# Optimization experiments

Hardware: AMD Instinct MI355X
Metric: run time of the kernel (lower is better)

Reference implementation:

```python
import jax, jax.numpy as jnp
import numpy as np

N = 100000
E = 1600000
K = 15        # kernel_size (num Gaussian mixture components)
DIM = 3       # pseudo-coordinate dim
EPS = 1e-15   # PyG GMMConv sigma epsilon
BN_EPS = 1e-5
CH = [(50, 75), (75, 100), (100, 75), (75, 50)]


def setup_inputs() -> dict:
    key = jax.random.key(0)
    ks = iter(jax.random.split(key, 64))
    inp = {}
    inp["x"] = jax.random.normal(next(ks), (N, 50), jnp.float32)
    inp["edge_index"] = jax.random.randint(next(ks), (2, E), 0, N, jnp.int64)
    inp["edge_attr"] = jax.random.uniform(next(ks), (E, DIM), jnp.float32)
    for l, (cin, cout) in enumerate(CH, 1):
        inp[f"g{l}"] = jax.random.normal(next(ks), (cin, K, cout), jnp.float32) * 0.1
        inp[f"mu{l}"] = jax.random.normal(next(ks), (K, DIM), jnp.float32)
        inp[f"sigma{l}"] = jnp.ones((K, DIM), jnp.float32) + 0.1 * jax.random.uniform(next(ks), (K, DIM), jnp.float32)
        inp[f"root{l}"] = jax.random.normal(next(ks), (cin, cout), jnp.float32) * 0.1
        inp[f"b{l}"] = jax.random.normal(next(ks), (cout,), jnp.float32) * 0.01
        if l < 4:
            inp[f"gamma{l}"] = jnp.ones((cout,), jnp.float32)
            inp[f"beta{l}"] = jnp.zeros((cout,), jnp.float32)
    return inp


def gmm_layer(x, src, tgt, pseudo, g, mu, sigma, root, bias):
    # Gaussian mixture edge weights: w[e,k] = exp(-0.5 * sum_d (u_ed - mu_kd)^2 / sigma_kd^2)
    n = x.shape[0]
    diff = pseudo[:, None, :] - mu[None, :, :]              # [E,K,dim]
    w = jnp.exp(-0.5 * jnp.sum(diff * diff / (sigma[None] ** 2 + EPS), axis=-1))  # [E,K]
    xs = x[src]                                             # gather source feats [E,Cin]
    # out_t = sum_k (sum_{e->t} w_ek * x_src[e]) @ G_k  (avoids [E,K,Cout] tensor)
    agg = jnp.zeros((n, g.shape[2]), x.dtype)
    for k in range(K):
        zk = jax.ops.segment_sum(xs * w[:, k:k + 1], tgt, num_segments=n)  # [N,Cin]
        agg = agg + zk @ g[:, k, :]
    deg = jax.ops.segment_sum(jnp.ones((src.shape[0],), x.dtype), tgt, num_segments=n)
    agg = agg / jnp.maximum(deg, 1.0)[:, None]              # aggr='mean'
    return agg + x @ root + bias


def batchnorm(x, gamma, beta):
    m = jnp.mean(x, axis=0)
    v = jnp.var(x, axis=0)
    return gamma * (x - m) * jax.lax.rsqrt(v + BN_EPS) + beta


def reference(x, edge_index, edge_attr,
              g1, mu1, sigma1, root1, b1, gamma1, beta1,
              g2, mu2, sigma2, root2, b2, gamma2, beta2,
              g3, mu3, sigma3, root3, b3, gamma3, beta3,
              g4, mu4, sigma4, root4, b4):
    src, tgt = edge_index[0], edge_index[1]
    h = jax.nn.elu(gmm_layer(x, src, tgt, edge_attr, g1, mu1, sigma1, root1, b1))
    h = batchnorm(h, gamma1, beta1)
    h = jax.nn.elu(gmm_layer(h, src, tgt, edge_attr, g2, mu2, sigma2, root2, b2))
    h = batchnorm(h, gamma2, beta2)
    h = jax.nn.elu(gmm_layer(h, src, tgt, edge_attr, g3, mu3, sigma3, root3, b3))
    h = batchnorm(h, gamma3, beta3)
    return gmm_layer(h, src, tgt, edge_attr, g4, mu4, sigma4, root4, b4)
```

## Files before the change

### kernel.cpp

```cpp
#include <hip/hip_runtime.h>
#include <stdint.h>

#define NN 100000
#define NE 1600000
#define KG 15

typedef unsigned short u16;
typedef __attribute__((ext_vector_type(8))) short short8;
typedef __attribute__((ext_vector_type(8))) __bf16 bf16x8;
typedef __attribute__((ext_vector_type(4))) float f32x4;

static __device__ __forceinline__ float bf2f(u16 u){ return __uint_as_float(((unsigned)u)<<16); }
static __device__ __forceinline__ u16 f2bf(float f){
  unsigned u = __float_as_uint(f);
  u += 0x7FFFu + ((u>>16)&1u);
  return (u16)(u>>16);
}
static __device__ __forceinline__ float ldf(const void* p, long long i, int isf32){
  return isf32 ? ((const float*)p)[i] : bf2f(((const u16*)p)[i]);
}
static __device__ __forceinline__ int ld_idx(const void* p, long long i, int isi64){
  return isi64 ? (int)((const long long*)p)[i] : ((const int*)p)[i];
}
static __device__ __forceinline__ f32x4 mfma16x16x32(short8 a, short8 b, f32x4 c){
  return __builtin_amdgcn_mfma_f32_16x16x32_bf16(
      __builtin_bit_cast(bf16x8, a), __builtin_bit_cast(bf16x8, b), c, 0, 0, 0);
}

__global__ void k_sentinel(float* out, float val){
  if (threadIdx.x == 0 && blockIdx.x == 0) out[0] = val;
}

__global__ void k_probe(const void* sg1, const void* ei, int* flags){
  if (threadIdx.x == 0 && blockIdx.x == 0){
    const u16* p = (const u16*)sg1;
    int sane = 1;
    for (int i=0;i<45;i++){ float v = bf2f(p[i]); if (!(v > 0.5f && v < 2.0f)) sane = 0; }
    flags[0] = sane ? 0 : 1;
    const int* q = (const int*)ei;
    int allz = 1;
    for (int i=1;i<128;i+=2) if (q[i] != 0) allz = 0;
    flags[1] = allz ? 1 : 0;
  }
}

__global__ __launch_bounds__(256) void k_convx(const void* x, u16* xcv, const int* flags){
  int i = blockIdx.x*256 + threadIdx.x;
  int c = i & 63, r = i >> 6;
  if (r >= NN) return;
  int isf = flags[0];
  u16 v = 0;
  if (c < 50){
    long long s = (long long)r*50 + c;
    v = isf ? f2bf(((const float*)x)[s]) : ((const u16*)x)[s];
  }
  xcv[(size_t)r*64 + c] = v;
}

__global__ __launch_bounds__(256) void k_deg(const void* ei, int* __restrict__ deg, const int* flags){
  int e = blockIdx.x*256 + threadIdx.x;
  int isi64 = flags[1];
  atomicAdd(&deg[ld_idx(ei, (long long)NE + e, isi64)], 1);
}

__global__ __launch_bounds__(256) void k_scan1(const int* __restrict__ deg, int* __restrict__ rp,
                                               int* __restrict__ bsum){
  __shared__ int lds[256];
  int b = blockIdx.x, t = threadIdx.x;
  int base = b*1024 + t*4;
  int v[4]; int s = 0;
  #pragma unroll
  for (int i=0;i<4;i++){ v[i] = (base+i < NN) ? deg[base+i] : 0; s += v[i]; }
  lds[t] = s; __syncthreads();
  int inc = s;
  for (int off=1; off<256; off<<=1){
    int y = (t>=off) ? lds[t-off] : 0;
    __syncthreads();
    inc += y; lds[t] = inc;
    __syncthreads();
  }
  int excl = inc - s;
  #pragma unroll
  for (int i=0;i<4;i++){ if (base+i < NN) rp[base+i] = excl; excl += v[i]; }
  if (t == 255) bsum[b] = inc;
}

__global__ __launch_bounds__(128) void k_scan2(int* __restrict__ bsum, int* __restrict__ rp){
  __shared__ int lds[128];
  int t = threadIdx.x;
  const int nb = (NN + 1023)/1024;
  int s = (t < nb) ? bsum[t] : 0;
  lds[t] = s; __syncthreads();
  int inc = s;
  for (int off=1; off<128; off<<=1){
    int y = (t>=off) ? lds[t-off] : 0;
    __syncthreads();
    inc += y; lds[t] = inc;
    __syncthreads();
  }
  bsum[t] = inc - s;
  if (t == 0) rp[NN] = NE;
}

__global__ __launch_bounds__(256) void k_scan3(int* __restrict__ rp, const int* __restrict__ bsum){
  int b = blockIdx.x, t = threadIdx.x;
  int add = bsum[b];
  int base = b*1024 + t*4;
  #pragma unroll
  for (int i=0;i<4;i++) if (base+i < NN) rp[base+i] += add;
}

__global__ __launch_bounds__(256) void k_fill(const void* ei, const void* attr,
                                              const int* __restrict__ rp, int* __restrict__ cur,
                                              int* __restrict__ perm, int4* __restrict__ csr16,
                                              int emode, const int* flags){
  int e = blockIdx.x*256 + threadIdx.x;
  int isf = flags[0], isi64 = flags[1];
  int t = ld_idx(ei, (long long)NE + e, isi64);
  int p = rp[t] + atomicAdd(&cur[t], 1);
  if (emode){
    int s = ld_idx(ei, e, isi64);
    float u0 = ldf(attr, 3LL*e+0, isf), u1 = ldf(attr, 3LL*e+1, isf), u2 = ldf(attr, 3LL*e+2, isf);
    csr16[p] = make_int4(s, __float_as_int(u0), __float_as_int(u1), __float_as_int(u2));
  } else {
    perm[p] = e;
  }
}

__global__ __launch_bounds__(256) void k_repack(const void* g, const void* root,
                                                u16* __restrict__ bp, int KC, int CIN, int COUT,
                                                int KS, int NCT, const int* flags){
  int tid = blockIdx.x*256 + threadIdx.x;
  int total = NCT*KS*64;
  if (tid >= total) return;
  int isf = flags[0];
  int lane = tid & 63;
  int ks = (tid >> 6) % KS;
  int ct = tid / (64*KS);
  int c = ct*16 + (lane & 15);
  int kbase = ks*32 + (lane >> 4)*8;
  short8 v8 = {};
  #pragma unroll
  for (int j=0;j<8;j++){
    int kk = kbase + j; u16 v = 0;
    if (c < COUT){
      if (kk < KC){
        int k = kk / CIN, cin = kk - k*CIN;
        v = f2bf(ldf(g, ((long long)cin*KG + k)*COUT + c, isf));
      } else if (kk < KC + CIN){
        v = f2bf(ldf(root, (long long)(kk-KC)*COUT + c, isf));
      }
    }
    v8[j] = (short)v;
  }
  ((short8*)bp)[tid] = v8;
}

template<int CIN, int COUT, int KPAD, int NCT, int XS, bool EM16, bool FINAL>
__global__ __launch_bounds__(512) void k_fused(
    const int4* __restrict__ csr16, const int* __restrict__ perm,
    const void* ei, const void* attr, const int* __restrict__ rp,
    const u16* __restrict__ xin, const void* mu, const void* sg,
    const u16* __restrict__ bp, const void* bias,
    u16* __restrict__ h, float* __restrict__ outp,
    float* __restrict__ sums, float* __restrict__ sumsq, const int* flags)
{
  constexpr int KC   = CIN*KG;
  constexpr int P    = (CIN + 31)/32;
  constexpr int NA   = 2*P;
  constexpr int RS   = KPAD + 8;
  constexpr int KS   = KPAD/32;
  __shared__ short8 zsh[16*RS/8];
  u16* zb = (u16*)zsh;

  int isf = flags[0], isi64 = flags[1];
  int wv = threadIdx.x >> 6, lane = threadIdx.x & 63;
  int m = lane & 15, q = lane >> 4;
  int node0 = blockIdx.x * 16;

  bool kvalid = (m < KG);
  int mm = kvalid ? m : 0;
  float mu0 = ldf(mu, mm*3+0, isf), mu1 = ldf(mu, mm*3+1, isf), mu2 = ldf(mu, mm*3+2, isf);
  float s0 = ldf(sg, mm*3+0, isf),  s1 = ldf(sg, mm*3+1, isf),  s2 = ldf(sg, mm*3+2, isf);
  float is0 = 1.f/(s0*s0 + 1e-15f), is1 = 1.f/(s1*s1 + 1e-15f), is2 = 1.f/(s2*s2 + 1e-15f);

  #pragma unroll 1
  for (int s = 0; s < 2; s++){
    int r = wv*2 + s;
    int t = node0 + r;
    int rs = rp[t], re = rp[t+1];
    f32x4 acc[NA] = {};
    int lastE = re - 1;
    for (int base = rs; base < re; base += 32){
      int e0 = base + q*8;
      int srcs[8];
      short8 af;
      {
        float u0[8], u1[8], u2[8];
        if (EM16){
          int4 ce[8];
          #pragma unroll
          for (int j=0;j<8;j++){
            int ep = e0 + j; ep = (ep > lastE) ? lastE : ep;
            ce[j] = csr16[ep];
          }
          #pragma unroll
          for (int j=0;j<8;j++){
            srcs[j] = ce[j].x;
            u0[j] = __int_as_float(ce[j].y); u1[j] = __int_as_float(ce[j].z); u2[j] = __int_as_float(ce[j].w);
          }
        } else {
          int eix[8];
          #pragma unroll
          for (int j=0;j<8;j++){
            int ep = e0 + j; ep = (ep > lastE) ? lastE : ep;
            eix[j] = perm[ep];
          }
          #pragma unroll
          for (int j=0;j<8;j++) srcs[j] = ld_idx(ei, eix[j], isi64);
          #pragma unroll
          for (int j=0;j<8;j++){
            u0[j] = ldf(attr, 3LL*eix[j]+0, isf);
            u1[j] = ldf(attr, 3LL*eix[j]+1, isf);
            u2[j] = ldf(attr, 3LL*eix[j]+2, isf);
          }
        }
        #pragma unroll
        for (int j=0;j<8;j++){
          float d0 = u0[j] - mu0, d1 = u1[j] - mu1, d2 = u2[j] - mu2;
          float w = __expf(-0.5f*(d0*d0*is0 + d1*d1*is1 + d2*d2*is2));
          bool ok = kvalid && (e0 + j <= lastE);
          w = ok ? w : 0.f;
          af[j] = (short)f2bf(w);
        }
      }

      unsigned xw[8*P];
      #pragma unroll
      for (int p=0; p<P; p++)
        #pragma unroll
        for (int j=0;j<8;j++)
          xw[p*8+j] = *(const unsigned*)(xin + (size_t)srcs[j]*XS + p*32 + 2*m);

      #pragma unroll
      for (int p=0; p<P; p++){
        int cin_e = p*32 + 2*m;
        bool ve = (cin_e < CIN), vo = (cin_e + 1 < CIN);
        short8 bfe, bfo;
        #pragma unroll
        for (int j=0;j<8;j++){
          bfe[j] = ve ? (short)(xw[p*8+j] & 0xffffu) : (short)0;
          bfo[j] = vo ? (short)(xw[p*8+j] >> 16) : (short)0;
        }
        acc[2*p]   = mfma16x16x32(af, bfe, acc[2*p]);
        acc[2*p+1] = mfma16x16x32(af, bfo, acc[2*p+1]);
      }
    }

    int dg = re - rs;
    float inv = 1.f / (float)(dg > 0 ? dg : 1);
    u16* row = zb + r*RS;
    #pragma unroll
    for (int ct=0; ct<NA; ct++){
      int cin = (ct>>1)*32 + 2*m + (ct&1);
      if (cin < CIN){
        #pragma unroll
        for (int rr=0;rr<4;rr++){
          int k = q*4 + rr;
          if (k < KG) row[k*CIN + cin] = f2bf(acc[ct][rr]*inv);
        }
      }
    }
    for (int idx = lane; idx < KPAD - KC; idx += 64){
      u16 v = 0;
      if (idx < CIN) v = xin[(size_t)t*XS + idx];
      row[KC + idx] = v;
    }
  }

  __syncthreads();

  if (wv < NCT){
    const short8* bpv = (const short8*)bp;
    const short8* zv  = (const short8*)zsh;
    f32x4 a0 = {}, a1 = {};
    #pragma unroll 2
    for (int ks=0; ks+1<KS; ks+=2){
      short8 af0 = zv[m*(RS/8) + ks*4 + q];
      short8 bf0 = bpv[(wv*KS + ks)*64 + lane];
      a0 = mfma16x16x32(af0, bf0, a0);
      short8 af1 = zv[m*(RS/8) + (ks+1)*4 + q];
      short8 bf1 = bpv[(wv*KS + ks+1)*64 + lane];
      a1 = mfma16x16x32(af1, bf1, a1);
    }
    if (KS & 1){
      short8 af0 = zv[m*(RS/8) + (KS-1)*4 + q];
      short8 bf0 = bpv[(wv*KS + KS-1)*64 + lane];
      a0 = mfma16x16x32(af0, bf0, a0);
    }
    f32x4 acc = a0 + a1;
    int col = wv*16 + m;
    if (col < COUT){
      float bv = ldf(bias, col, isf);
      float vs[4];
      #pragma unroll
      for (int rr=0;rr<4;rr++){
        int rrow = node0 + q*4 + rr;
        float v = acc[rr] + bv;
        if (!FINAL){
          v = (v > 0.f) ? v : (__expf(v) - 1.f);
          vs[rr] = v;
          h[(size_t)rrow*COUT + col] = f2bf(v);
        } else {
          outp[(size_t)rrow*COUT + col] = v;
        }
      }
      if (!FINAL){
        float ss = vs[0]+vs[1]+vs[2]+vs[3];
        float qq = vs[0]*vs[0]+vs[1]*vs[1]+vs[2]*vs[2]+vs[3]*vs[3];
        ss += __shfl_xor(ss, 16); ss += __shfl_xor(ss, 32);
        qq += __shfl_xor(qq, 16); qq += __shfl_xor(qq, 32);
        if (q == 0){
          atomicAdd(&sums[col], ss);
          atomicAdd(&sumsq[col], qq);
        }
      }
    }
  }
}

__global__ __launch_bounds__(256) void k_bn(const u16* __restrict__ h, const void* gamma,
                                            const void* beta, const float* __restrict__ sums,
                                            const float* __restrict__ sumsq, u16* __restrict__ xo,
                                            int COUT, const int* flags){
  int t = threadIdx.x;
  int isf = flags[0];
  int c = t & 127;
  int r = blockIdx.x*2 + (t >> 7);
  if (r >= NN) return;
  if (c >= COUT){
    if (c < 128) xo[(size_t)r*128 + c] = 0;
    return;
  }
  const float invn = 1.f/(float)NN;
  float mean = sums[c]*invn;
  float var  = sumsq[c]*invn - mean*mean;
  float g = ldf(gamma, c, isf), b = ldf(beta, c, isf);
  float v = g*(bf2f(h[(size_t)r*COUT + c]) - mean)*rsqrtf(var + 1e-5f) + b;
  xo[(size_t)r*128 + c] = f2bf(v);
}

extern "C" void kernel_launch(void* const* d_in, const int* in_sizes, int n_in,
                              void* d_out, int out_size, void* d_ws, size_t ws_size,
                              hipStream_t stream)
{
  static const int expected[29] = {
    5000000, 3200000, 4800000,
    56250, 45, 45, 3750, 75, 75, 75,
    112500, 45, 45, 7500, 100, 100, 100,
    112500, 45, 45, 7500, 75, 75, 75,
    56250, 45, 45, 3750, 50
  };
  if (n_in != 29){ k_sentinel<<<1, 64, 0, stream>>>((float*)d_out, 512.0f); return; }
  for (int j=0;j<29;j++){
    if (in_sizes[j] != expected[j]){
      k_sentinel<<<1, 64, 0, stream>>>((float*)d_out, 1024.0f*(float)(1+j));
      return;
    }
  }

  const void* x0   = d_in[0];
  const void* ei   = d_in[1];
  const void* attr = d_in[2];
  const void* G[4]  = {d_in[3],  d_in[10], d_in[17], d_in[24]};
  const void* MU[4] = {d_in[4],  d_in[11], d_in[18], d_in[25]};
  const void* SG[4] = {d_in[5],  d_in[12], d_in[19], d_in[26]};
  const void* RT[4] = {d_in[6],  d_in[13], d_in[20], d_in[27]};
  const void* BI[4] = {d_in[7],  d_in[14], d_in[21], d_in[28]};
  const void* GA[3] = {d_in[8],  d_in[15], d_in[22]};
  const void* BE[3] = {d_in[9],  d_in[16], d_in[23]};

  char* w = (char*)d_ws;
  auto alloc = [&](size_t bytes)->char*{ char* p = w; w += (bytes + 255) & ~(size_t)255; return p; };
  int*  flags = (int*) alloc(256);
  int*  deg  = (int*) alloc((size_t)NN*4);
  int*  cur  = (int*) alloc((size_t)NN*4);
  int*  rp   = (int*) alloc((size_t)(NN+1)*4);
  int*  bsum = (int*) alloc(512*4);
  u16*  h    = (u16*) alloc((size_t)NN*100*2);
  u16*  xb   = (u16*) alloc((size_t)NN*128*2);
  u16*  bp   = (u16*) alloc(1<<19);
  float* sums  = (float*)alloc(512);
  float* sumsq = (float*)alloc(512);
  u16*  xcv  = xb + (size_t)NN*64;

  size_t base = (size_t)(w - (char*)d_ws);
  int emode; int* perm = nullptr; int4* csr16 = nullptr;
  if (ws_size >= base + (size_t)NE*16 + 4096){
    emode = 1; csr16 = (int4*)alloc((size_t)NE*16);
  } else if (ws_size >= base + (size_t)NE*4 + 4096){
    emode = 0; perm = (int*)alloc((size_t)NE*4);
  } else {
    float mb = (float)(ws_size >> 20); if (mb > 255.f) mb = 255.f;
    k_sentinel<<<1, 64, 0, stream>>>((float*)d_out, 65536.0f + 256.0f*mb);
    return;
  }

  k_probe<<<1, 64, 0, stream>>>(SG[0], ei, flags);
  k_convx<<<NN*64/256, 256, 0, stream>>>(x0, xcv, flags);

  hipMemsetAsync(deg, 0, (size_t)NN*4, stream);
  hipMemsetAsync(cur, 0, (size_t)NN*4, stream);
  k_deg  <<<NE/256, 256, 0, stream>>>(ei, deg, flags);
  k_scan1<<<(NN+1023)/1024, 256, 0, stream>>>(deg, rp, bsum);
  k_scan2<<<1, 128, 0, stream>>>(bsum, rp);
  k_scan3<<<(NN+1023)/1024, 256, 0, stream>>>(rp, bsum);
  k_fill <<<NE/256, 256, 0, stream>>>(ei, attr, rp, cur, perm, csr16, emode, flags);

  const int NB = NN/16;

  {
    k_repack<<<(5*25*64 + 255)/256, 256, 0, stream>>>(G[0], RT[0], bp, 750, 50, 75, 25, 5, flags);
    hipMemsetAsync(sums, 0, 512, stream); hipMemsetAsync(sumsq, 0, 512, stream);
    if (emode) k_fused<50,75,800,5,64,true ,false><<<NB,512,0,stream>>>(csr16, perm, ei, attr, rp, xcv, MU[0], SG[0], bp, BI[0], h, nullptr, sums, sumsq, flags);
    else       k_fused<50,75,800,5,64,false,false><<<NB,512,0,stream>>>(csr16, perm, ei, attr, rp, xcv, MU[0], SG[0], bp, BI[0], h, nullptr, sums, sumsq, flags);
    k_bn<<<NN/2, 256, 0, stream>>>(h, GA[0], BE[0], sums, sumsq, xb, 75, flags);
  }

  {
    k_repack<<<(7*38*64 + 255)/256, 256, 0, stream>>>(G[1], RT[1], bp, 1125, 75, 100, 38, 7, flags);
    hipMemsetAsync(sums, 0, 512, stream); hipMemsetAsync(sumsq, 0, 512, stream);
    if (emode) k_fused<75,100,1216,7,128,true ,false><<<NB,512,0,stream>>>(csr16, perm, ei, attr, rp, xb, MU[1], SG[1], bp, BI[1], h, nullptr, sums, sumsq, flags);
    else       k_fused<75,100,1216,7,128,false,false><<<NB,512,0,stream>>>(csr16, perm, ei, attr, rp, xb, MU[1], SG[1], bp, BI[1], h, nullptr, sums, sumsq, flags);
    k_bn<<<NN/2, 256, 0, stream>>>(h, GA[1], BE[1], sums, sumsq, xb, 100, flags);
  }

  {
    k_repack<<<(5*50*64 + 255)/256, 256, 0, stream>>>(G[2], RT[2], bp, 1500, 100, 75, 50, 5, flags);
    hipMemsetAsync(sums, 0, 512, stream); hipMemsetAsync(sumsq, 0, 512, stream);
    if (emode) k_fused<100,75,1600,5,128,true ,false><<<NB,512,0,stream>>>(csr16, perm, ei, attr, rp, xb, MU[2], SG[2], bp, BI[2], h, nullptr, sums, sumsq, flags);
    else       k_fused<100,75,1600,5,128,false,false><<<NB,512,0,stream>>>(csr16, perm, ei, attr, rp, xb, MU[2], SG[2], bp, BI[2], h, nullptr, sums, sumsq, flags);
    k_bn<<<NN/2, 256, 0, stream>>>(h, GA[2], BE[2], sums, sumsq, xb, 75, flags);
  }

  {
    k_repack<<<(4*38*64 + 255)/256, 256, 0, stream>>>(G[3], RT[3], bp, 1125, 75, 50, 38, 4, flags);
    if (emode) k_fused<75,50,1216,4,128,true ,true><<<NB,512,0,stream>>>(csr16, perm, ei, attr, rp, xb, MU[3], SG[3], bp, BI[3], nullptr, (float*)d_out, sums, sumsq, flags);
    else       k_fused<75,50,1216,4,128,false,true><<<NB,512,0,stream>>>(csr16, perm, ei, attr, rp, xb, MU[3], SG[3], bp, BI[3], nullptr, (float*)d_out, sums, sumsq, flags);
  }
}
```

Measured before the change: 1.117 ms.

## Split node features into 64-column main buffer plus compact tail buffer

The single 128-column padded bf16 feature buffer is replaced by a 64-column main array and a separate tail array whose stride matches the layer width (16 for 75 channels, 64 for 100). The goal is to shrink the gathered working set per source node and improve cache-line density and L2 hit rate in the edge gather. Edge CSR reads and the h/output writes also get nontemporal hints so streaming data does not evict the reused features. This adds a per-chunk branch on which buffer to read. It relies on masking to ignore the now-uninitialised tail padding.

```diff
diff --git a/kernel.cpp b/kernel.cpp
--- a/kernel.cpp
+++ b/kernel.cpp
@@ -9,6 +9,7 @@
 typedef __attribute__((ext_vector_type(8))) short short8;
 typedef __attribute__((ext_vector_type(8))) __bf16 bf16x8;
 typedef __attribute__((ext_vector_type(4))) float f32x4;
+typedef __attribute__((ext_vector_type(4))) int i32x4;
 
 static __device__ __forceinline__ float bf2f(u16 u){ return __uint_as_float(((unsigned)u)<<16); }
 static __device__ __forceinline__ u16 f2bf(float f){
@@ -44,7 +45,7 @@
   }
 }
 
-__global__ __launch_bounds__(256) void k_convx(const void* x, u16* xcv, const int* flags){
+__global__ __launch_bounds__(256) void k_convx(const void* x, u16* xm, const int* flags){
   int i = blockIdx.x*256 + threadIdx.x;
   int c = i & 63, r = i >> 6;
   if (r >= NN) return;
@@ -54,7 +55,7 @@
     long long s = (long long)r*50 + c;
     v = isf ? f2bf(((const float*)x)[s]) : ((const u16*)x)[s];
   }
-  xcv[(size_t)r*64 + c] = v;
+  xm[(size_t)r*64 + c] = v;
 }
 
 __global__ __launch_bounds__(256) void k_deg(const void* ei, int* __restrict__ deg, const int* flags){
@@ -156,11 +157,12 @@
   ((short8*)bp)[tid] = v8;
 }
 
-template<int CIN, int COUT, int KPAD, int NCT, int XS, bool EM16, bool FINAL>
+template<int CIN, int COUT, int KPAD, int NCT, int TS, bool EM16, bool FINAL>
 __global__ __launch_bounds__(512) void k_fused(
     const int4* __restrict__ csr16, const int* __restrict__ perm,
     const void* ei, const void* attr, const int* __restrict__ rp,
-    const u16* __restrict__ xin, const void* mu, const void* sg,
+    const u16* __restrict__ xin, const u16* __restrict__ xtl,
+    const void* mu, const void* sg,
     const u16* __restrict__ bp, const void* bias,
     u16* __restrict__ h, float* __restrict__ outp,
     float* __restrict__ sums, float* __restrict__ sumsq, const int* flags)
@@ -198,23 +200,23 @@
       {
         float u0[8], u1[8], u2[8];
         if (EM16){
-          int4 ce[8];
+          i32x4 ce[8];
           #pragma unroll
           for (int j=0;j<8;j++){
             int ep = e0 + j; ep = (ep > lastE) ? lastE : ep;
-            ce[j] = csr16[ep];
+            ce[j] = __builtin_nontemporal_load((const i32x4*)&csr16[ep]);
           }
           #pragma unroll
           for (int j=0;j<8;j++){
-            srcs[j] = ce[j].x;
-            u0[j] = __int_as_float(ce[j].y); u1[j] = __int_as_float(ce[j].z); u2[j] = __int_as_float(ce[j].w);
+            srcs[j] = ce[j][0];
+            u0[j] = __int_as_float(ce[j][1]); u1[j] = __int_as_float(ce[j][2]); u2[j] = __int_as_float(ce[j][3]);
           }
         } else {
           int eix[8];
           #pragma unroll
           for (int j=0;j<8;j++){
             int ep = e0 + j; ep = (ep > lastE) ? lastE : ep;
-            eix[j] = perm[ep];
+            eix[j] = __builtin_nontemporal_load(&perm[ep]);
           }
           #pragma unroll
           for (int j=0;j<8;j++) srcs[j] = ld_idx(ei, eix[j], isi64);
@@ -239,8 +241,11 @@
       #pragma unroll
       for (int p=0; p<P; p++)
         #pragma unroll
-        for (int j=0;j<8;j++)
-          xw[p*8+j] = *(const unsigned*)(xin + (size_t)srcs[j]*XS + p*32 + 2*m);
+        for (int j=0;j<8;j++){
+          const u16* bpt = (p < 2) ? (xin + (size_t)srcs[j]*64 + p*32 + 2*m)
+                                   : (xtl + (size_t)srcs[j]*TS + (p-2)*32 + 2*m);
+          xw[p*8+j] = *(const unsigned*)bpt;
+        }
 
       #pragma unroll
       for (int p=0; p<P; p++){
@@ -273,7 +278,7 @@
     }
     for (int idx = lane; idx < KPAD - KC; idx += 64){
       u16 v = 0;
-      if (idx < CIN) v = xin[(size_t)t*XS + idx];
+      if (idx < CIN) v = (idx < 64) ? xin[(size_t)t*64 + idx] : xtl[(size_t)t*TS + idx - 64];
       row[KC + idx] = v;
     }
   }
@@ -310,9 +315,9 @@
         if (!FINAL){
           v = (v > 0.f) ? v : (__expf(v) - 1.f);
           vs[rr] = v;
-          h[(size_t)rrow*COUT + col] = f2bf(v);
+          __builtin_nontemporal_store(f2bf(v), &h[(size_t)rrow*COUT + col]);
         } else {
-          outp[(size_t)rrow*COUT + col] = v;
+          __builtin_nontemporal_store(v, &outp[(size_t)rrow*COUT + col]);
         }
       }
       if (!FINAL){
@@ -331,23 +336,22 @@
 
 __global__ __launch_bounds__(256) void k_bn(const u16* __restrict__ h, const void* gamma,
                                             const void* beta, const float* __restrict__ sums,
-                                            const float* __restrict__ sumsq, u16* __restrict__ xo,
-                                            int COUT, const int* flags){
+                                            const float* __restrict__ sumsq,
+                                            u16* __restrict__ xm, u16* __restrict__ xt,
+                                            int TS, int COUT, const int* flags){
   int t = threadIdx.x;
   int isf = flags[0];
   int c = t & 127;
   int r = blockIdx.x*2 + (t >> 7);
-  if (r >= NN) return;
-  if (c >= COUT){
-    if (c < 128) xo[(size_t)r*128 + c] = 0;
-    return;
-  }
+  if (r >= NN || c >= COUT) return;
   const float invn = 1.f/(float)NN;
   float mean = sums[c]*invn;
   float var  = sumsq[c]*invn - mean*mean;
   float g = ldf(gamma, c, isf), b = ldf(beta, c, isf);
   float v = g*(bf2f(h[(size_t)r*COUT + c]) - mean)*rsqrtf(var + 1e-5f) + b;
-  xo[(size_t)r*128 + c] = f2bf(v);
+  u16 o = f2bf(v);
+  if (c < 64) xm[(size_t)r*64 + c] = o;
+  else        xt[(size_t)r*TS + c - 64] = o;
 }
 
 extern "C" void kernel_launch(void* const* d_in, const int* in_sizes, int n_in,
@@ -388,11 +392,12 @@
   int*  rp   = (int*) alloc((size_t)(NN+1)*4);
   int*  bsum = (int*) alloc(512*4);
   u16*  h    = (u16*) alloc((size_t)NN*100*2);
-  u16*  xb   = (u16*) alloc((size_t)NN*128*2);
+  u16*  xmain= (u16*) alloc((size_t)NN*64*2);
+  u16*  xt75 = (u16*) alloc((size_t)NN*16*2 + 512);
+  u16*  xt100= (u16*) alloc((size_t)NN*64*2 + 512);
   u16*  bp   = (u16*) alloc(1<<19);
   float* sums  = (float*)alloc(512);
   float* sumsq = (float*)alloc(512);
-  u16*  xcv  = xb + (size_t)NN*64;
 
   size_t base = (size_t)(w - (char*)d_ws);
   int emode; int* perm = nullptr; int4* csr16 = nullptr;
@@ -407,7 +412,7 @@
   }
 
   k_probe<<<1, 64, 0, stream>>>(SG[0], ei, flags);
-  k_convx<<<NN*64/256, 256, 0, stream>>>(x0, xcv, flags);
+  k_convx<<<NN*64/256, 256, 0, stream>>>(x0, xmain, flags);
 
   hipMemsetAsync(deg, 0, (size_t)NN*4, stream);
   hipMemsetAsync(cur, 0, (size_t)NN*4, stream);
@@ -422,30 +427,30 @@
   {
     k_repack<<<(5*25*64 + 255)/256, 256, 0, stream>>>(G[0], RT[0], bp, 750, 50, 75, 25, 5, flags);
     hipMemsetAsync(sums, 0, 512, stream); hipMemsetAsync(sumsq, 0, 512, stream);
-    if (emode) k_fused<50,75,800,5,64,true ,false><<<NB,512,0,stream>>>(csr16, perm, ei, attr, rp, xcv, MU[0], SG[0], bp, BI[0], h, nullptr, sums, sumsq, flags);
-    else       k_fused<50,75,800,5,64,false,false><<<NB,512,0,stream>>>(csr16, perm, ei, attr, rp, xcv, MU[0], SG[0], bp, BI[0], h, nullptr, sums, sumsq, flags);
-    k_bn<<<NN/2, 256, 0, stream>>>(h, GA[0], BE[0], sums, sumsq, xb, 75, flags);
+    if (emode) k_fused<50,75,800,5,16,true ,false><<<NB,512,0,stream>>>(csr16, perm, ei, attr, rp, xmain, xt75, MU[0], SG[0], bp, BI[0], h, nullptr, sums, sumsq, flags);
+    else       k_fused<50,75,800,5,16,false,false><<<NB,512,0,stream>>>(csr16, perm, ei, attr, rp, xmain, xt75, MU[0], SG[0], bp, BI[0], h, nullptr, sums, sumsq, flags);
+    k_bn<<<NN/2, 256, 0, stream>>>(h, GA[0], BE[0], sums, sumsq, xmain, xt75, 16, 75, flags);
   }
 
   {
     k_repack<<<(7*38*64 + 255)/256, 256, 0, stream>>>(G[1], RT[1], bp, 1125, 75, 100, 38, 7, flags);
     hipMemsetAsync(sums, 0, 512, stream); hipMemsetAsync(sumsq, 0, 512, stream);
-    if (emode) k_fused<75,100,1216,7,128,true ,false><<<NB,512,0,stream>>>(csr16, perm, ei, attr, rp, xb, MU[1], SG[1], bp, BI[1], h, nullptr, sums, sumsq, flags);
-    else       k_fused<75,100,1216,7,128,false,false><<<NB,512,0,stream>>>(csr16, perm, ei, attr, rp, xb, MU[1], SG[1], bp, BI[1], h, nullptr, sums, sumsq, flags);
-    k_bn<<<NN/2, 256, 0, stream>>>(h, GA[1], BE[1], sums, sumsq, xb, 100, flags);
+    if (emode) k_fused<75,100,1216,7,16,true ,false><<<NB,512,0,stream>>>(csr16, perm, ei, attr, rp, xmain, xt75, MU[1], SG[1], bp, BI[1], h, nullptr, sums, sumsq, flags);
+    else       k_fused<75,100,1216,7,16,false,false><<<NB,512,0,stream>>>(csr16, perm, ei, attr, rp, xmain, xt75, MU[1], SG[1], bp, BI[1], h, nullptr, sums, sumsq, flags);
+    k_bn<<<NN/2, 256, 0, stream>>>(h, GA[1], BE[1], sums, sumsq, xmain, xt100, 64, 100, flags);
   }
 
   {
     k_repack<<<(5*50*64 + 255)/256, 256, 0, stream>>>(G[2], RT[2], bp, 1500, 100, 75, 50, 5, flags);
     hipMemsetAsync(sums, 0, 512, stream); hipMemsetAsync(sumsq, 0, 512, stream);
-    if (emode) k_fused<100,75,1600,5,128,true ,false><<<NB,512,0,stream>>>(csr16, perm, ei, attr, rp, xb, MU[2], SG[2], bp, BI[2], h, nullptr, sums, sumsq, flags);
-    else       k_fused<100,75,1600,5,128,false,false><<<NB,512,0,stream>>>(csr16, perm, ei, attr, rp, xb, MU[2], SG[2], bp, BI[2], h, nullptr, sums, sumsq, flags);
-    k_bn<<<NN/2, 256, 0, stream>>>(h, GA[2], BE[2], sums, sumsq, xb, 75, flags);
+    if (emode) k_fused<100,75,1600,5,64,true ,false><<<NB,512,0,stream>>>(csr16, perm, ei, attr, rp, xmain, xt100, MU[2], SG[2], bp, BI[2], h, nullptr, sums, sumsq, flags);
+    else       k_fused<100,75,1600,5,64,false,false><<<NB,512,0,stream>>>(csr16, perm, ei, attr, rp, xmain, xt100, MU[2], SG[2], bp, BI[2], h, nullptr, sums, sumsq, flags);
+    k_bn<<<NN/2, 256, 0, stream>>>(h, GA[2], BE[2], sums, sumsq, xmain, xt75, 16, 75, flags);
   }
 
   {
     k_repack<<<(4*38*64 + 255)/256, 256, 0, stream>>>(G[3], RT[3], bp, 1125, 75, 50, 38, 4, flags);
-    if (emode) k_fused<75,50,1216,4,128,true ,true><<<NB,512,0,stream>>>(csr16, perm, ei, attr, rp, xb, MU[3], SG[3], bp, BI[3], nullptr, (float*)d_out, sums, sumsq, flags);
-    else       k_fused<75,50,1216,4,128,false,true><<<NB,512,0,stream>>>(csr16, perm, ei, attr, rp, xb, MU[3], SG[3], bp, BI[3], nullptr, (float*)d_out, sums, sumsq, flags);
-  }
-}
+    if (emode) k_fused<75,50,1216,4,16,true ,true><<<NB,512,0,stream>>>(csr16, perm, ei, attr, rp, xmain, xt75, MU[3], SG[3], bp, BI[3], nullptr, (float*)d_out, sums, sumsq, flags);
+    else       k_fused<75,50,1216,4,16,false,true><<<NB,512,0,stream>>>(csr16, perm, ei, attr, rp, xmain, xt75, MU[3], SG[3], bp, BI[3], nullptr, (float*)d_out, sums, sumsq, flags);
+  }
+}
```

Result: slower. 1.216 ms (+8.9%).
